# Kernel tuning notes

Measured on AMD Instinct MI355X. Metric: run time of the kernel, lower is better.

Reference implementation:

```python
import jax, jax.numpy as jnp
import numpy as np

BETA_MAX = 5.0


def setup_inputs() -> dict:
    key = jax.random.key(0)
    ks = jax.random.split(key, 10)
    N, M, R, d, NTAU, G = 100000, 1000000, 4, 16, 16, 128
    return {
        "c_3": jax.random.randint(ks[0], (M,), 0, N),
        "u_3": jax.random.randint(ks[1], (M,), 0, N),
        "v_3": jax.random.randint(ks[2], (M,), 0, N),
        "t_tau": jax.random.randint(ks[3], (M,), 0, NTAU),
        "batch": jnp.sort(jax.random.randint(ks[4], (N,), 0, G)),
        "Q3": jax.random.normal(ks[5], (N, R, d), dtype=jnp.float32),
        "K3": jax.random.normal(ks[6], (N, R, d), dtype=jnp.float32),
        "T_params": jax.random.normal(ks[7], (NTAU, d), dtype=jnp.float32),
        "raw_lambda_3": jax.random.uniform(ks[8], (1,), dtype=jnp.float32),
        "raw_beta_3": jax.random.uniform(ks[9], (1,), dtype=jnp.float32),
        "num_nodes": N,
        "num_graphs": G,
    }


def reference(c_3, u_3, v_3, t_tau, batch, Q3, K3, T_params,
              raw_lambda_3, raw_beta_3, num_nodes, num_graphs):
    R, d = Q3.shape[-2], Q3.shape[-1]
    scale = (R * d) ** 0.5
    lam = jax.nn.softplus(raw_lambda_3[0])            # positive_param
    beta = jnp.minimum(jax.nn.softplus(raw_beta_3[0]), BETA_MAX)  # inverse_temperature

    # fused motif dot: gather Q/K by triangle indices, contract over d -> [M, R]
    T_sel = T_params[t_tau]                           # [M, d]
    ell = jnp.einsum('mrd,mrd,mrd,md->mr', Q3[c_3], K3[u_3], K3[v_3], T_sel) / scale
    z = beta * ell                                    # [M, R]

    # segment logsumexp over center-node segments c_3 -> [num_nodes, R]
    seg_max = jax.ops.segment_max(z, c_3, num_segments=num_nodes)
    safe_max = jnp.where(jnp.isfinite(seg_max), seg_max, 0.0)
    sums = jax.ops.segment_sum(jnp.exp(z - safe_max[c_3]), c_3, num_segments=num_nodes)
    lse = jnp.where(sums > 0, safe_max + jnp.log(jnp.where(sums > 0, sums, 1.0)), 0.0)

    # scatter-add node lse into graphs -> [num_graphs, R]
    graph_lse = jax.ops.segment_sum(lse, batch, num_segments=num_graphs)
    return (lam / beta) * graph_lse
```

## Files before the change

kernel.cpp:

```cpp
#include <hip/hip_runtime.h>


#define RR 4
#define DD 16
#define BETA_MAX 5.0f

__device__ __forceinline__ float softplus_f(float x) {
    return log1pf(__expf(x));
}

__global__ void me_init(const float* __restrict__ raw_lam,
                        const float* __restrict__ raw_beta,
                        float* __restrict__ scal, float* __restrict__ sums,
                        float* __restrict__ out, int nr, int out_size) {
    int i = blockIdx.x * blockDim.x + threadIdx.x;
    if (i == 0) {
        float beta = fminf(softplus_f(raw_beta[0]), BETA_MAX);
        float lam  = softplus_f(raw_lam[0]);
        scal[0] = beta * 0.125f;
        scal[1] = lam / beta;
    }
    if (i < nr) sums[i] = 0.0f;
    if (i < out_size) out[i] = 0.0f;
}

__global__ void me_motif(const int* __restrict__ c3, const int* __restrict__ u3,
                         const int* __restrict__ v3, const int* __restrict__ tt,
                         const float* __restrict__ Q3, const float* __restrict__ K3,
                         const float* __restrict__ Tp, const float* __restrict__ scal,
                         float* __restrict__ sums, int M) {
    int tid = blockIdx.x * blockDim.x + threadIdx.x;
    int m = tid >> 4;
    if (m >= M) return;
    int l  = tid & 15;
    int r  = l >> 2;
    int dc = (l & 3) << 2;

    int c = c3[m], u = u3[m], v = v3[m], t = tt[m];
    float bscale = scal[0];

    const float4 q  = *(const float4*)(Q3 + ((size_t)c * (RR * DD) + r * DD + dc));
    const float4 ku = *(const float4*)(K3 + ((size_t)u * (RR * DD) + r * DD + dc));
    const float4 kv = *(const float4*)(K3 + ((size_t)v * (RR * DD) + r * DD + dc));
    const float4 tw = *(const float4*)(Tp + ((size_t)t * DD + dc));

    float p = q.x * ku.x * kv.x * tw.x + q.y * ku.y * kv.y * tw.y +
              q.z * ku.z * kv.z * tw.z + q.w * ku.w * kv.w * tw.w;
    p += __shfl_xor(p, 1);
    p += __shfl_xor(p, 2);

    if ((l & 3) == 0) {
        float z = bscale * p;
        atomicAdd(&sums[c * RR + r], __expf(z));
    }
}

__global__ void me_node(const float* __restrict__ sums, const int* __restrict__ batch,
                        const float* __restrict__ scal, float* __restrict__ out,
                        int N, int out_size) {
    extern __shared__ float acc[];
    for (int i = threadIdx.x; i < out_size; i += blockDim.x) acc[i] = 0.0f;
    __syncthreads();

    int tid = blockIdx.x * blockDim.x + threadIdx.x;
    if (tid < N * RR) {
        int n = tid >> 2, r = tid & 3;
        float s = sums[tid];
        if (s > 0.0f) {
            float lse = logf(s);
            int g = batch[n];
            atomicAdd(&acc[g * RR + r], lse);
        }
    }
    __syncthreads();

    float coef = scal[1];
    for (int i = threadIdx.x; i < out_size; i += blockDim.x) {
        float a = acc[i];
        if (a != 0.0f) atomicAdd(&out[i], a * coef);
    }
}

extern "C" void kernel_launch(void* const* d_in, const int* in_sizes, int n_in,
                              void* d_out, int out_size, void* d_ws, size_t ws_size,
                              hipStream_t stream) {
    const int*   c3    = (const int*)d_in[0];
    const int*   u3    = (const int*)d_in[1];
    const int*   v3    = (const int*)d_in[2];
    const int*   tt    = (const int*)d_in[3];
    const int*   batch = (const int*)d_in[4];
    const float* Q3    = (const float*)d_in[5];
    const float* K3    = (const float*)d_in[6];
    const float* Tp    = (const float*)d_in[7];
    const float* rlam  = (const float*)d_in[8];
    const float* rbeta = (const float*)d_in[9];

    const int M  = in_sizes[0];
    const int N  = in_sizes[5] / (RR * DD);
    const int nr = N * RR;

    float* scal = (float*)d_ws;
    float* sums = scal + 2;
    float* out  = (float*)d_out;

    {
        int tot = nr > out_size ? nr : out_size;
        me_init<<<(tot + 255) / 256, 256, 0, stream>>>(rlam, rbeta, scal, sums, out, nr, out_size);
    }
    {
        long long threads = (long long)M * 16;
        int blocks = (int)((threads + 255) / 256);
        me_motif<<<blocks, 256, 0, stream>>>(c3, u3, v3, tt, Q3, K3, Tp, scal, sums, M);
    }
    {
        int blocks = (nr + 255) / 256;
        me_node<<<blocks, 256, (size_t)out_size * sizeof(float), stream>>>(
            sums, batch, scal, out, N, out_size);
    }
}
```

Baseline: 216.4 us.

## Convert Q3/K3 to fp16 copies and gather half-precision rows in motif kernel

```diff
diff --git a/kernel.cpp b/kernel.cpp
--- a/kernel.cpp
+++ b/kernel.cpp
@@ -1,18 +1,25 @@
 #include <hip/hip_runtime.h>
+#include <hip/hip_fp16.h>
 
 
 #define RR 4
 #define DD 16
 #define BETA_MAX 5.0f
 
+struct __attribute__((aligned(16))) h8 { __half2 h[4]; };
+
 __device__ __forceinline__ float softplus_f(float x) {
     return log1pf(__expf(x));
 }
 
-__global__ void me_init(const float* __restrict__ raw_lam,
-                        const float* __restrict__ raw_beta,
-                        float* __restrict__ scal, float* __restrict__ sums,
-                        float* __restrict__ out, int nr, int out_size) {
+__global__ void me_init_convert(const float* __restrict__ raw_lam,
+                                const float* __restrict__ raw_beta,
+                                const float* __restrict__ Q3,
+                                const float* __restrict__ K3,
+                                h8* __restrict__ Qh, h8* __restrict__ Kh,
+                                float* __restrict__ scal, float* __restrict__ sums,
+                                float* __restrict__ out,
+                                int n8each, int nr, int out_size) {
     int i = blockIdx.x * blockDim.x + threadIdx.x;
     if (i == 0) {
         float beta = fminf(softplus_f(raw_beta[0]), BETA_MAX);
@@ -22,26 +29,79 @@
     }
     if (i < nr) sums[i] = 0.0f;
     if (i < out_size) out[i] = 0.0f;
-}
-
-__global__ void me_motif(const int* __restrict__ c3, const int* __restrict__ u3,
-                         const int* __restrict__ v3, const int* __restrict__ tt,
-                         const float* __restrict__ Q3, const float* __restrict__ K3,
-                         const float* __restrict__ Tp, const float* __restrict__ scal,
-                         float* __restrict__ sums, int M) {
+    if (i < 2 * n8each) {
+        const float* src = (i < n8each) ? Q3 : K3;
+        h8*          dst = (i < n8each) ? Qh : Kh;
+        int j = (i < n8each) ? i : i - n8each;
+        float4 a = ((const float4*)src)[2 * j];
+        float4 b = ((const float4*)src)[2 * j + 1];
+        h8 o;
+        o.h[0] = __halves2half2(__float2half_rn(a.x), __float2half_rn(a.y));
+        o.h[1] = __halves2half2(__float2half_rn(a.z), __float2half_rn(a.w));
+        o.h[2] = __halves2half2(__float2half_rn(b.x), __float2half_rn(b.y));
+        o.h[3] = __halves2half2(__float2half_rn(b.z), __float2half_rn(b.w));
+        dst[j] = o;
+    }
+}
+
+__global__ void me_motif_h(const int* __restrict__ c3, const int* __restrict__ u3,
+                           const int* __restrict__ v3, const int* __restrict__ tt,
+                           const h8* __restrict__ Qh, const h8* __restrict__ Kh,
+                           const float* __restrict__ Tp, const float* __restrict__ scal,
+                           float* __restrict__ sums, int M) {
+    int tid = blockIdx.x * blockDim.x + threadIdx.x;
+    int m = tid >> 3;
+    if (m >= M) return;
+    int l = tid & 7;
+    int r = l >> 1;
+    int dc = (l & 1) << 3;
+
+    int c = c3[m], u = u3[m], v = v3[m], t = tt[m];
+    float bscale = scal[0];
+
+    h8 q  = Qh[(size_t)c * 8 + l];
+    h8 ku = Kh[(size_t)u * 8 + l];
+    h8 kv = Kh[(size_t)v * 8 + l];
+    const float4 t0 = *(const float4*)(Tp + t * DD + dc);
+    const float4 t1 = *(const float4*)(Tp + t * DD + dc + 4);
+
+    float2 qf, uf, vf;
+    float p = 0.0f;
+    qf = __half22float2(q.h[0]); uf = __half22float2(ku.h[0]); vf = __half22float2(kv.h[0]);
+    p += qf.x * uf.x * vf.x * t0.x + qf.y * uf.y * vf.y * t0.y;
+    qf = __half22float2(q.h[1]); uf = __half22float2(ku.h[1]); vf = __half22float2(kv.h[1]);
+    p += qf.x * uf.x * vf.x * t0.z + qf.y * uf.y * vf.y * t0.w;
+    qf = __half22float2(q.h[2]); uf = __half22float2(ku.h[2]); vf = __half22float2(kv.h[2]);
+    p += qf.x * uf.x * vf.x * t1.x + qf.y * uf.y * vf.y * t1.y;
+    qf = __half22float2(q.h[3]); uf = __half22float2(ku.h[3]); vf = __half22float2(kv.h[3]);
+    p += qf.x * uf.x * vf.x * t1.z + qf.y * uf.y * vf.y * t1.w;
+
+    p += __shfl_xor(p, 1);
+
+    if ((l & 1) == 0) {
+        atomicAdd(&sums[c * RR + r], __expf(bscale * p));
+    }
+}
+
+__global__ void me_motif_f32(const int* __restrict__ c3, const int* __restrict__ u3,
+                             const int* __restrict__ v3, const int* __restrict__ tt,
+                             const float* __restrict__ Q3, const float* __restrict__ K3,
+                             const float* __restrict__ Tp, const float* __restrict__ scal,
+                             float* __restrict__ sums, int M) {
     int tid = blockIdx.x * blockDim.x + threadIdx.x;
     int m = tid >> 4;
     if (m >= M) return;
-    int l  = tid & 15;
-    int r  = l >> 2;
-    int dc = (l & 3) << 2;
+    int l = tid & 15;
+    int r = l >> 2;
+    int off = r * DD + ((l & 3) << 2);
+    int dc  = (l & 3) << 2;
 
     int c = c3[m], u = u3[m], v = v3[m], t = tt[m];
     float bscale = scal[0];
 
-    const float4 q  = *(const float4*)(Q3 + ((size_t)c * (RR * DD) + r * DD + dc));
-    const float4 ku = *(const float4*)(K3 + ((size_t)u * (RR * DD) + r * DD + dc));
-    const float4 kv = *(const float4*)(K3 + ((size_t)v * (RR * DD) + r * DD + dc));
+    const float4 q  = *(const float4*)(Q3 + ((size_t)c * (RR * DD) + off));
+    const float4 ku = *(const float4*)(K3 + ((size_t)u * (RR * DD) + off));
+    const float4 kv = *(const float4*)(K3 + ((size_t)v * (RR * DD) + off));
     const float4 tw = *(const float4*)(Tp + ((size_t)t * DD + dc));
 
     float p = q.x * ku.x * kv.x * tw.x + q.y * ku.y * kv.y * tw.y +
@@ -49,10 +109,22 @@
     p += __shfl_xor(p, 1);
     p += __shfl_xor(p, 2);
 
-    if ((l & 3) == 0) {
-        float z = bscale * p;
-        atomicAdd(&sums[c * RR + r], __expf(z));
-    }
+    if ((l & 3) == 0) atomicAdd(&sums[c * RR + r], __expf(bscale * p));
+}
+
+__global__ void me_init_f32(const float* __restrict__ raw_lam,
+                            const float* __restrict__ raw_beta,
+                            float* __restrict__ scal, float* __restrict__ sums,
+                            float* __restrict__ out, int nr, int out_size) {
+    int i = blockIdx.x * blockDim.x + threadIdx.x;
+    if (i == 0) {
+        float beta = fminf(softplus_f(raw_beta[0]), BETA_MAX);
+        float lam  = softplus_f(raw_lam[0]);
+        scal[0] = beta * 0.125f;
+        scal[1] = lam / beta;
+    }
+    if (i < nr) sums[i] = 0.0f;
+    if (i < out_size) out[i] = 0.0f;
 }
 
 __global__ void me_node(const float* __restrict__ sums, const int* __restrict__ batch,
@@ -62,15 +134,12 @@
     for (int i = threadIdx.x; i < out_size; i += blockDim.x) acc[i] = 0.0f;
     __syncthreads();
 
-    int tid = blockIdx.x * blockDim.x + threadIdx.x;
-    if (tid < N * RR) {
+    int total = N * RR;
+    for (int tid = blockIdx.x * blockDim.x + threadIdx.x; tid < total;
+         tid += gridDim.x * blockDim.x) {
         int n = tid >> 2, r = tid & 3;
         float s = sums[tid];
-        if (s > 0.0f) {
-            float lse = logf(s);
-            int g = batch[n];
-            atomicAdd(&acc[g * RR + r], lse);
-        }
+        if (s > 0.0f) atomicAdd(&acc[batch[n] * RR + r], logf(s));
     }
     __syncthreads();
 
@@ -95,26 +164,49 @@
     const float* rlam  = (const float*)d_in[8];
     const float* rbeta = (const float*)d_in[9];
 
-    const int M  = in_sizes[0];
-    const int N  = in_sizes[5] / (RR * DD);
-    const int nr = N * RR;
-
-    float* scal = (float*)d_ws;
-    float* sums = scal + 2;
-    float* out  = (float*)d_out;
-
-    {
-        int tot = nr > out_size ? nr : out_size;
-        me_init<<<(tot + 255) / 256, 256, 0, stream>>>(rlam, rbeta, scal, sums, out, nr, out_size);
-    }
-    {
-        long long threads = (long long)M * 16;
-        int blocks = (int)((threads + 255) / 256);
-        me_motif<<<blocks, 256, 0, stream>>>(c3, u3, v3, tt, Q3, K3, Tp, scal, sums, M);
-    }
-    {
-        int blocks = (nr + 255) / 256;
-        me_node<<<blocks, 256, (size_t)out_size * sizeof(float), stream>>>(
+    const int M   = in_sizes[0];
+    const int nel = in_sizes[5];
+    const int N   = nel / (RR * DD);
+    const int nr  = N * RR;
+
+    const size_t half_bytes = (size_t)nel * sizeof(__half);
+    const size_t need = 2 * half_bytes + (2 + (size_t)nr) * sizeof(float);
+
+    float* out = (float*)d_out;
+
+    if (ws_size >= need) {
+        h8*    Qh   = (h8*)d_ws;
+        h8*    Kh   = (h8*)((char*)d_ws + half_bytes);
+        float* scal = (float*)((char*)d_ws + 2 * half_bytes);
+        float* sums = scal + 2;
+
+        const int n8each = nel / 8;
+        {
+            int tot = 2 * n8each;
+            if (nr > tot) tot = nr;
+            me_init_convert<<<(tot + 255) / 256, 256, 0, stream>>>(
+                rlam, rbeta, Q3, K3, Qh, Kh, scal, sums, out, n8each, nr, out_size);
+        }
+        {
+            long long threads = (long long)M * 8;
+            int blocks = (int)((threads + 255) / 256);
+            me_motif_h<<<blocks, 256, 0, stream>>>(c3, u3, v3, tt, Qh, Kh, Tp, scal, sums, M);
+        }
+        me_node<<<256, 256, (size_t)out_size * sizeof(float), stream>>>(
             sums, batch, scal, out, N, out_size);
-    }
-}
+    } else {
+        float* scal = (float*)d_ws;
+        float* sums = scal + 2;
+        {
+            int tot = nr > out_size ? nr : out_size;
+            me_init_f32<<<(tot + 255) / 256, 256, 0, stream>>>(rlam, rbeta, scal, sums, out, nr, out_size);
+        }
+        {
+            long long threads = (long long)M * 16;
+            int blocks = (int)((threads + 255) / 256);
+            me_motif_f32<<<blocks, 256, 0, stream>>>(c3, u3, v3, tt, Q3, K3, Tp, scal, sums, M);
+        }
+        me_node<<<256, 256, (size_t)out_size * sizeof(float), stream>>>(
+            sums, batch, scal, out, N, out_size);
+    }
+}
```

New measurement: 191.7 us. 11.4% less time.
